# Kernel tuning notes

Hardware: AMD Instinct MI355X
Metric: run time of the kernel (lower is better)

## Reference

```python
import jax, jax.numpy as jnp
import numpy as np

B, S, E = 8, 2048, 2048   # batch, items, embedding_width
H, Dh = 16, 128           # head_width, head_embeddings (E = H*Dh)
M = 1024                  # memory_width


def setup_inputs() -> dict:
    key = jax.random.key(0)
    ks = jax.random.split(key, 9)
    scale_e = 1.0 / np.sqrt(E)
    scale_d = 1.0 / np.sqrt(Dh)
    return {
        "tensor": jax.random.normal(ks[0], (B, S, E), dtype=jnp.float32),
        # Query: Linear(E -> [H, Dh])
        "Wq": jax.random.normal(ks[1], (E, H, Dh), dtype=jnp.float32) * scale_e,
        "bq": jnp.zeros((H, Dh), dtype=jnp.float32),
        # trainable key/value banks + calibration (kaiming-uniform-like init)
        "key_params": (jax.random.uniform(ks[2], (H, M, Dh), dtype=jnp.float32) * 2 - 1) * np.sqrt(6.0 / Dh),
        "calibration": jnp.zeros((H, M, Dh), dtype=jnp.float32),
        "value": (jax.random.uniform(ks[3], (H, M, Dh), dtype=jnp.float32) * 2 - 1) * np.sqrt(6.0 / Dh),
        # Dehead: Linear([H, Dh] -> E)
        "Wd": jax.random.normal(ks[4], (H, Dh, E), dtype=jnp.float32) * scale_d,
        "bd": jnp.zeros((E,), dtype=jnp.float32),
    }


def reference(tensor, Wq, bq, key_params, calibration, value, Wd, bd):
    # query projection to heads: (B,S,E) -> (B,H,S,Dh) (fuses transpose(-2,-3))
    q = jnp.einsum("bse,ehd->bhsd", tensor, Wq) + bq[:, None, :]
    # eval-mode dropout is identity; key = KeyParameters + CalibrationBuffer
    k = key_params + calibration                      # (H,M,Dh)
    # scores scaled by sqrt(FULL embedding width), per the source
    score = jnp.einsum("bhsd,hmd->bhsm", q, k) / jnp.sqrt(jnp.float32(E))
    attn = jax.nn.softmax(score, axis=-1)             # (B,H,S,M)
    out = jnp.einsum("bhsm,hmd->bhsd", attn, value)   # (B,H,S,Dh)
    # dehead: (B,H,S,Dh) -> (B,S,E)
    return jnp.einsum("bhsd,hde->bse", out, Wd) + bd
```

## Files before the change

### kernel.cpp

```cpp
#include <hip/hip_runtime.h>
#include <stdint.h>

#define B_ 8
#define S_ 2048
#define E_ 2048
#define H_ 16
#define DH_ 128
#define M_ 1024
#define K_ 2048

typedef float f32x4 __attribute__((ext_vector_type(4)));
typedef float f32x16 __attribute__((ext_vector_type(16)));
typedef __bf16 bf16x8 __attribute__((ext_vector_type(8)));
typedef unsigned short ushort8 __attribute__((ext_vector_type(8)));
typedef unsigned short ushort4v __attribute__((ext_vector_type(4)));
typedef unsigned int uint4v __attribute__((ext_vector_type(4)));
typedef float float4v __attribute__((ext_vector_type(4)));

static __device__ __forceinline__ unsigned short f2bf(float f) {
  unsigned int u = __builtin_bit_cast(unsigned int, f);
  u += 0x7fffu + ((u >> 16) & 1u);
  return (unsigned short)(u >> 16);
}

static __device__ __forceinline__ float exp2f_fast(float x) {
#if __has_builtin(__builtin_amdgcn_exp2f)
  return __builtin_amdgcn_exp2f(x);
#else
  return __expf(x * 0.6931471805599453f);
#endif
}

static __device__ __forceinline__ f32x4 mfma16(ushort8 a, ushort8 b, f32x4 c) {
  return __builtin_amdgcn_mfma_f32_16x16x32_bf16(
      __builtin_bit_cast(bf16x8, a), __builtin_bit_cast(bf16x8, b), c, 0, 0, 0);
}

static __device__ __forceinline__ f32x16 mfma32(ushort8 a, ushort8 b, f32x16 c) {
  return __builtin_amdgcn_mfma_f32_32x32x16_bf16(
      __builtin_bit_cast(bf16x8, a), __builtin_bit_cast(bf16x8, b), c, 0, 0, 0);
}

static __device__ __forceinline__ void gload_lds16(const void* g, void* l) {
  __builtin_amdgcn_global_load_lds(
      (const __attribute__((address_space(1))) unsigned int*)g,
      (__attribute__((address_space(3))) unsigned int*)l, 16, 0, 0);
}


__global__ void cvt_bf16(const float* __restrict__ in, unsigned short* __restrict__ out, int n4) {
  int i = blockIdx.x * blockDim.x + threadIdx.x;
  int stride = gridDim.x * blockDim.x;
  for (; i < n4; i += stride) {
    float4v v = ((const float4v*)in)[i];
    ushort4v o;
    o[0] = f2bf(v[0]); o[1] = f2bf(v[1]); o[2] = f2bf(v[2]); o[3] = f2bf(v[3]);
    ((ushort4v*)out)[i] = o;
  }
}

__global__ void addcvt_bf16(const float* __restrict__ a, const float* __restrict__ b,
                            unsigned short* __restrict__ out, int n4) {
  int i = blockIdx.x * blockDim.x + threadIdx.x;
  int stride = gridDim.x * blockDim.x;
  for (; i < n4; i += stride) {
    float4v va = ((const float4v*)a)[i];
    float4v vb = ((const float4v*)b)[i];
    ushort4v o;
    o[0] = f2bf(va[0] + vb[0]); o[1] = f2bf(va[1] + vb[1]);
    o[2] = f2bf(va[2] + vb[2]); o[3] = f2bf(va[3] + vb[3]);
    ((ushort4v*)out)[i] = o;
  }
}

__global__ __launch_bounds__(256) void transpose_cvt(const float* __restrict__ in,
                                                     unsigned short* __restrict__ out,
                                                     int R, int C) {
  __shared__ float t[64][65];
  const int tx = threadIdx.x & 63, ty = threadIdx.x >> 6;
  const size_t base = (size_t)blockIdx.z * R * C;
  const int r0 = blockIdx.y * 64, c0 = blockIdx.x * 64;
#pragma unroll
  for (int i = 0; i < 64; i += 4)
    t[i + ty][tx] = in[base + (size_t)(r0 + i + ty) * C + (c0 + tx)];
  __syncthreads();
#pragma unroll
  for (int i = 0; i < 64; i += 4)
    out[base + (size_t)(c0 + i + ty) * R + (r0 + tx)] = f2bf(t[tx][i + ty]);
}

template <int EPI>
__global__ __launch_bounds__(512, 2) void gemm8p(const unsigned short* __restrict__ A,
                                                 const unsigned short* __restrict__ BT,
                                                 const float* __restrict__ bias,
                                                 void* __restrict__ Cout) {
  __shared__ __align__(16) unsigned short a_lds[2][2][8192];
  __shared__ __align__(16) unsigned short b_lds[2][2][8192];
  const int tid = threadIdx.x;
  const int w = tid >> 6, lane = tid & 63;
  const int l16 = lane & 15, l4 = lane >> 4;
  const int wr = w >> 2, wc = w & 3;
  const int bid = blockIdx.x;
  const int n0 = (bid & 7) << 8;
  const int m0 = (bid >> 3) << 8;

  const int rp0 = tid >> 3, gg0 = tid & 7, s0 = gg0 ^ (rp0 & 7);
  const int srow = rp0 * 2 + (s0 >> 2), sg = s0 & 3;
  const unsigned short* pA = A + (size_t)(m0 + srow) * K_ + sg * 8;
  const unsigned short* pB = BT + (size_t)(n0 + srow) * K_ + sg * 8;
  const int laneG = ((l16 >> 1) * 8 + (((l16 & 1) * 4 + l4) ^ ((l16 >> 1) & 7))) * 8;

  f32x4 acc[8][4];
#pragma unroll
  for (int i = 0; i < 8; ++i)
#pragma unroll
    for (int j = 0; j < 4; ++j) acc[i][j] = (f32x4)(0.f);

  ushort8 aF[4], bF[4];

#define STG(dst, srcp, T, kh)                                                \
  do {                                                                       \
    const unsigned short* s_ = (srcp) + (T) * 64 + (kh) * 32;                \
    gload_lds16(s_, &(dst)[tid * 8]);                                        \
    gload_lds16(s_ + (size_t)128 * K_, &(dst)[(512 + tid) * 8]);             \
  } while (0)

#define LDA(mg, buf, ks)                                                     \
  do {                                                                       \
    _Pragma("unroll") for (int mf = 0; mf < 4; ++mf)                         \
      aF[mf] = *(const ushort8*)&a_lds[buf][ks]                              \
          [(wr * 512 + ((mg) * 4 + mf) * 64) * 8 + laneG];                   \
  } while (0)

#define LDB(buf, ks)                                                         \
  do {                                                                       \
    _Pragma("unroll") for (int nf = 0; nf < 4; ++nf)                         \
      bF[nf] = *(const ushort8*)&b_lds[buf][ks]                              \
          [(wc * 256 + nf * 64) * 8 + laneG];                                \
  } while (0)

#define MM(mg)                                                               \
  do {                                                                       \
    __builtin_amdgcn_s_setprio(1);                                           \
    _Pragma("unroll") for (int mf = 0; mf < 4; ++mf)                         \
      _Pragma("unroll") for (int nf = 0; nf < 4; ++nf)                       \
        acc[(mg) * 4 + mf][nf] = mfma16(aF[mf], bF[nf], acc[(mg) * 4 + mf][nf]); \
    __builtin_amdgcn_s_setprio(0);                                           \
  } while (0)

#define NOVM ((void)0)
#define VMC6 asm volatile("s_waitcnt vmcnt(6)" ::: "memory")
#define VMC0 asm volatile("s_waitcnt vmcnt(0)" ::: "memory")

#define PHASE(mg, ks, buf, LOADB, STAGE, VM)                                 \
  do {                                                                       \
    if (LOADB) { LDB(buf, ks); }                                             \
    LDA(mg, buf, ks);                                                        \
    STAGE;                                                                   \
    __builtin_amdgcn_s_barrier();                                            \
    asm volatile("s_waitcnt lgkmcnt(0)" ::: "memory");                       \
    __builtin_amdgcn_sched_barrier(0);                                       \
    MM(mg);                                                                  \
    VM;                                                                      \
    __builtin_amdgcn_s_barrier();                                            \
  } while (0)

  STG(a_lds[0][0], pA, 0, 0);
  STG(b_lds[0][0], pB, 0, 0);
  STG(a_lds[0][1], pA, 0, 1);
  STG(b_lds[0][1], pB, 0, 1);
  STG(b_lds[1][0], pB, 1, 0);
  STG(a_lds[1][0], pA, 1, 0);
  STG(b_lds[1][1], pB, 1, 1);
  __builtin_amdgcn_sched_barrier(0);
  VMC6;
  __builtin_amdgcn_s_barrier();
  __builtin_amdgcn_sched_barrier(0);

#pragma unroll 1
  for (int i = 0; i < 15; ++i) {
    const int t1 = 2 * i + 1, t2 = 2 * i + 2, t3 = 2 * i + 3;
    PHASE(0, 0, 0, 1, STG(a_lds[1][1], pA, t1, 1), NOVM);
    PHASE(1, 0, 0, 0, STG(b_lds[0][0], pB, t2, 0), NOVM);
    PHASE(1, 1, 0, 1, STG(a_lds[0][0], pA, t2, 0), NOVM);
    PHASE(0, 1, 0, 0, STG(b_lds[0][1], pB, t2, 1), VMC6);
    PHASE(0, 0, 1, 1, STG(a_lds[0][1], pA, t2, 1), NOVM);
    PHASE(1, 0, 1, 0, STG(b_lds[1][0], pB, t3, 0), NOVM);
    PHASE(1, 1, 1, 1, STG(a_lds[1][0], pA, t3, 0), NOVM);
    PHASE(0, 1, 1, 0, STG(b_lds[1][1], pB, t3, 1), VMC6);
  }
  PHASE(0, 0, 0, 1, STG(a_lds[1][1], pA, 31, 1), NOVM);
  PHASE(1, 0, 0, 0, NOVM, NOVM);
  PHASE(1, 1, 0, 1, NOVM, NOVM);
  PHASE(0, 1, 0, 0, NOVM, VMC0);
  PHASE(0, 0, 1, 1, NOVM, NOVM);
  PHASE(1, 0, 1, 0, NOVM, NOVM);
  PHASE(1, 1, 1, 1, NOVM, NOVM);
  PHASE(0, 1, 1, 0, NOVM, NOVM);

#undef PHASE
#undef STG
#undef LDA
#undef LDB
#undef MM

#pragma unroll
  for (int mf = 0; mf < 8; ++mf) {
    const int mb = m0 + wr * 128 + mf * 16 + l4 * 4;
#pragma unroll
    for (int nf = 0; nf < 4; ++nf) {
      const int n = n0 + wc * 64 + nf * 16 + l16;
      const float bv = bias[n];
#pragma unroll
      for (int r = 0; r < 4; ++r) {
        const float v = acc[mf][nf][r] + bv;
        const int m = mb + r;
        if (EPI == 0) {
          const int b = m >> 11, s = m & 2047, h = n >> 7, d = n & 127;
          ((unsigned short*)Cout)[(((size_t)(b * 16 + h) << 11) + s) * 128 + d] =
              f2bf(v * 0.031879358f);
        } else {
          ((float*)Cout)[(size_t)m * E_ + n] = v;
        }
      }
    }
  }
}

__global__ __launch_bounds__(512, 2) void attnY(const unsigned short* __restrict__ Qb,
                                                const unsigned short* __restrict__ Kb,
                                                const unsigned short* __restrict__ VT,
                                                unsigned short* __restrict__ Ob) {
  const int bh = blockIdx.x, b = bh >> 4, h = bh & 15;
  const int tid = threadIdx.x, wv = tid >> 6, lane = tid & 63;
  const int l32 = lane & 31, hi = lane >> 5;
  const int rg = wv >> 1, dh = wv & 1;

  __shared__ __align__(16) unsigned short k_sm[2][16 * 512];
  __shared__ __align__(16) unsigned short v_sm[2][16 * 512];
  __shared__ float inv_lds[8][2][32];

  const unsigned short* Kh = Kb + (size_t)h * M_ * DH_;
  const unsigned short* Vh = VT + (size_t)h * DH_ * M_;

  ushort8 qf[2][8];
  const int srow0 = blockIdx.y * 256 + rg * 64;
#pragma unroll
  for (int sub = 0; sub < 2; ++sub) {
    const unsigned short* qrow =
        Qb + ((size_t)(b * 16 + h) * S_ + srow0 + sub * 32 + l32) * DH_ + hi * 8;
#pragma unroll
    for (int dc = 0; dc < 8; ++dc) qf[sub][dc] = *(const ushort8*)(qrow + dc * 16);
  }

  f32x16 oacc[2][2];
#pragma unroll
  for (int sub = 0; sub < 2; ++sub)
#pragma unroll
    for (int dt = 0; dt < 2; ++dt) oacc[sub][dt] = (f32x16)(0.f);
  float lsum[2] = {0.f, 0.f};

#define ASTAGE(buf, ch)                                                         \
  do {                                                                          \
    const int m0c = (ch) << 6;                                                  \
    _Pragma("unroll") for (int j_ = 0; j_ < 2; ++j_) {                          \
      const int L_ = j_ * 512 + tid;                                            \
      const int st_ = L_ >> 6, g_ = L_ & 63;                                    \
      const int mb_ = st_ >> 3, dc_ = st_ & 7;                                  \
      const int pt_ = g_ >> 5, rw_ = g_ & 31;                                   \
      gload_lds16(Kh + (size_t)(m0c + mb_ * 32 + rw_) * DH_ + dc_ * 16 + pt_ * 8, \
                  &k_sm[buf][L_ * 8]);                                          \
    }                                                                           \
    _Pragma("unroll") for (int j_ = 0; j_ < 2; ++j_) {                          \
      const int L_ = j_ * 512 + tid;                                            \
      const int st_ = L_ >> 6, g_ = L_ & 63;                                    \
      const int dt_ = st_ >> 2, mb_ = (st_ >> 1) & 1, mk_ = st_ & 1;            \
      const int pt_ = g_ >> 5, rw_ = g_ & 31;                                   \
      gload_lds16(Vh + (size_t)(dt_ * 32 + rw_) * M_ + m0c + mb_ * 32 + mk_ * 16 + pt_ * 8, \
                  &v_sm[buf][L_ * 8]);                                          \
    }                                                                           \
  } while (0)

  int cur = 0;
  ASTAGE(0, 0);
  __syncthreads();

  for (int c = 0; c < 16; ++c) {
    if (c < 15) ASTAGE(cur ^ 1, c + 1);

#pragma unroll
    for (int mb = 0; mb < 2; ++mb) {
      f32x16 sacc0 = (f32x16)(0.f), sacc1 = (f32x16)(0.f);
      __builtin_amdgcn_s_setprio(1);
#pragma unroll
      for (int dc = 0; dc < 8; ++dc) {
        ushort8 kf = *(const ushort8*)&k_sm[cur][((mb * 8 + dc) * 64 + lane) * 8];
        sacc0 = mfma32(kf, qf[0][dc], sacc0);
        sacc1 = mfma32(kf, qf[1][dc], sacc1);
      }
      __builtin_amdgcn_s_setprio(0);

      ushort8 pa[2][2];
#pragma unroll
      for (int sub = 0; sub < 2; ++sub) {
        float pe[16];
#pragma unroll
        for (int r = 0; r < 16; ++r) {
          pe[r] = exp2f_fast(sub == 0 ? sacc0[r] : sacc1[r]);
          lsum[sub] += pe[r];
        }
#pragma unroll
        for (int mk = 0; mk < 2; ++mk) {
          const int o = mk * 8;
          unsigned x0, x1, y0, y1;
          asm("v_cvt_pk_bf16_f32 %0, %1, %2" : "=v"(x0) : "v"(pe[o + 0]), "v"(pe[o + 1]));
          asm("v_cvt_pk_bf16_f32 %0, %1, %2" : "=v"(x1) : "v"(pe[o + 2]), "v"(pe[o + 3]));
          asm("v_cvt_pk_bf16_f32 %0, %1, %2" : "=v"(y0) : "v"(pe[o + 4]), "v"(pe[o + 5]));
          asm("v_cvt_pk_bf16_f32 %0, %1, %2" : "=v"(y1) : "v"(pe[o + 6]), "v"(pe[o + 7]));
          asm("v_permlane32_swap_b32 %0, %1" : "+v"(x0), "+v"(y0));
          asm("v_permlane32_swap_b32 %0, %1" : "+v"(x1), "+v"(y1));
          uint4v pw;
          pw[0] = x0; pw[1] = x1; pw[2] = y0; pw[3] = y1;
          pa[sub][mk] = __builtin_bit_cast(ushort8, pw);
        }
      }

      __builtin_amdgcn_s_setprio(1);
#pragma unroll
      for (int dt = 0; dt < 2; ++dt) {
#pragma unroll
        for (int mk = 0; mk < 2; ++mk) {
          const int vst = (dh * 2 + dt) * 4 + mb * 2 + mk;
          ushort8 vf = *(const ushort8*)&v_sm[cur][(vst * 64 + lane) * 8];
          oacc[0][dt] = mfma32(pa[0][mk], vf, oacc[0][dt]);
          oacc[1][dt] = mfma32(pa[1][mk], vf, oacc[1][dt]);
        }
      }
      __builtin_amdgcn_s_setprio(0);
    }
    __syncthreads();
    cur ^= 1;
  }
#undef ASTAGE

#pragma unroll
  for (int sub = 0; sub < 2; ++sub) {
    float tot = lsum[sub] + __shfl_xor(lsum[sub], 32, 64);
    if (hi == 0) inv_lds[wv][sub][l32] = 1.0f / tot;
  }
  __builtin_amdgcn_s_barrier();
#pragma unroll
  for (int sub = 0; sub < 2; ++sub)
#pragma unroll
    for (int r = 0; r < 16; ++r) {
      const int crow = (r & 3) + 8 * (r >> 2) + 4 * hi;
      const float iv = inv_lds[wv][sub][crow];
      unsigned short* orow =
          Ob + ((size_t)b * S_ + (size_t)(srow0 + sub * 32 + crow)) * (H_ * DH_) +
          h * DH_ + dh * 64 + l32;
#pragma unroll
      for (int dt = 0; dt < 2; ++dt) {
        const float val = oacc[sub][dt][r] * iv;
        unsigned u;
        asm("v_cvt_pk_bf16_f32 %0, %1, %2" : "=v"(u) : "v"(val), "v"(val));
        orow[dt * 32] = (unsigned short)u;
      }
    }
}


extern "C" void kernel_launch(void* const* d_in, const int* in_sizes, int n_in,
                              void* d_out, int out_size, void* d_ws, size_t ws_size,
                              hipStream_t stream) {
  const float* X   = (const float*)d_in[0];
  const float* Wq  = (const float*)d_in[1];
  const float* bq  = (const float*)d_in[2];
  const float* Kp  = (const float*)d_in[3];
  const float* Cal = (const float*)d_in[4];
  const float* V   = (const float*)d_in[5];
  const float* Wd  = (const float*)d_in[6];
  const float* bd  = (const float*)d_in[7];

  char* ws = (char*)d_ws;
  unsigned short* Xbf = (unsigned short*)(ws + 0);
  unsigned short* Ob  = Xbf;
  unsigned short* Qb  = (unsigned short*)(ws + 67108864);
  unsigned short* WqT = (unsigned short*)(ws + 134217728);
  unsigned short* WdT = (unsigned short*)(ws + 142606336);
  unsigned short* Kb  = (unsigned short*)(ws + 150994944);
  unsigned short* VT  = (unsigned short*)(ws + 155189248);

  cvt_bf16<<<2048, 256, 0, stream>>>(X, Xbf, (B_ * S_ * E_) / 4);
  addcvt_bf16<<<1024, 256, 0, stream>>>(Kp, Cal, Kb, (H_ * M_ * DH_) / 4);
  transpose_cvt<<<dim3(E_ / 64, E_ / 64, 1), 256, 0, stream>>>(Wq, WqT, E_, H_ * DH_);
  transpose_cvt<<<dim3(E_ / 64, E_ / 64, 1), 256, 0, stream>>>(Wd, WdT, H_ * DH_, E_);
  transpose_cvt<<<dim3(DH_ / 64, M_ / 64, H_), 256, 0, stream>>>(V, VT, M_, DH_);

  gemm8p<0><<<dim3(512), 512, 0, stream>>>(Xbf, WqT, bq, Qb);

  attnY<<<dim3(B_ * H_, S_ / 256), 512, 0, stream>>>(Qb, Kb, VT, Ob);

  gemm8p<1><<<dim3(512), 512, 0, stream>>>(Ob, WdT, bd, (float*)d_out);
}
```

Before: 574.6 us.

## Repartition attention waves to own full head dim, removing duplicated score computation

Each wave now owns 32 query rows across the full 128-wide head dimension, instead of 64 rows over half the head dimension. Previously two waves computed identical QK^T scores and exponentials for the same rows. The new split computes scores and softmax exponentials once per row. The trade is less register reuse of V fragments, since each V read now feeds one MFMA instead of two, so LDS traffic per output rises.

Result: faster. 509.3 us (-11.4%).

```diff
diff --git a/kernel.cpp b/kernel.cpp
--- a/kernel.cpp
+++ b/kernel.cpp
@@ -227,38 +227,33 @@
   }
 }
 
-__global__ __launch_bounds__(512, 2) void attnY(const unsigned short* __restrict__ Qb,
+__global__ __launch_bounds__(512, 2) void attnZ(const unsigned short* __restrict__ Qb,
                                                 const unsigned short* __restrict__ Kb,
                                                 const unsigned short* __restrict__ VT,
                                                 unsigned short* __restrict__ Ob) {
   const int bh = blockIdx.x, b = bh >> 4, h = bh & 15;
   const int tid = threadIdx.x, wv = tid >> 6, lane = tid & 63;
   const int l32 = lane & 31, hi = lane >> 5;
-  const int rg = wv >> 1, dh = wv & 1;
+  const int s_glob = blockIdx.y * 256 + wv * 32 + l32;
 
   __shared__ __align__(16) unsigned short k_sm[2][16 * 512];
   __shared__ __align__(16) unsigned short v_sm[2][16 * 512];
-  __shared__ float inv_lds[8][2][32];
+  __shared__ float inv_lds[8][32];
 
   const unsigned short* Kh = Kb + (size_t)h * M_ * DH_;
   const unsigned short* Vh = VT + (size_t)h * DH_ * M_;
 
-  ushort8 qf[2][8];
-  const int srow0 = blockIdx.y * 256 + rg * 64;
-#pragma unroll
-  for (int sub = 0; sub < 2; ++sub) {
-    const unsigned short* qrow =
-        Qb + ((size_t)(b * 16 + h) * S_ + srow0 + sub * 32 + l32) * DH_ + hi * 8;
-#pragma unroll
-    for (int dc = 0; dc < 8; ++dc) qf[sub][dc] = *(const ushort8*)(qrow + dc * 16);
-  }
-
-  f32x16 oacc[2][2];
-#pragma unroll
-  for (int sub = 0; sub < 2; ++sub)
-#pragma unroll
-    for (int dt = 0; dt < 2; ++dt) oacc[sub][dt] = (f32x16)(0.f);
-  float lsum[2] = {0.f, 0.f};
+  ushort8 qf[8];
+  {
+    const unsigned short* qrow = Qb + ((size_t)(b * 16 + h) * S_ + s_glob) * DH_ + hi * 8;
+#pragma unroll
+    for (int dc = 0; dc < 8; ++dc) qf[dc] = *(const ushort8*)(qrow + dc * 16);
+  }
+
+  f32x16 oacc[4];
+#pragma unroll
+  for (int dt = 0; dt < 4; ++dt) oacc[dt] = (f32x16)(0.f);
+  float lsum = 0.f;
 
 #define ASTAGE(buf, ch)                                                         \
   do {                                                                          \
@@ -290,50 +285,45 @@
 
 #pragma unroll
     for (int mb = 0; mb < 2; ++mb) {
-      f32x16 sacc0 = (f32x16)(0.f), sacc1 = (f32x16)(0.f);
+      f32x16 sacc = (f32x16)(0.f);
       __builtin_amdgcn_s_setprio(1);
 #pragma unroll
       for (int dc = 0; dc < 8; ++dc) {
         ushort8 kf = *(const ushort8*)&k_sm[cur][((mb * 8 + dc) * 64 + lane) * 8];
-        sacc0 = mfma32(kf, qf[0][dc], sacc0);
-        sacc1 = mfma32(kf, qf[1][dc], sacc1);
+        sacc = mfma32(kf, qf[dc], sacc);
       }
       __builtin_amdgcn_s_setprio(0);
 
-      ushort8 pa[2][2];
-#pragma unroll
-      for (int sub = 0; sub < 2; ++sub) {
-        float pe[16];
-#pragma unroll
-        for (int r = 0; r < 16; ++r) {
-          pe[r] = exp2f_fast(sub == 0 ? sacc0[r] : sacc1[r]);
-          lsum[sub] += pe[r];
-        }
+      float pe[16];
+#pragma unroll
+      for (int r = 0; r < 16; ++r) {
+        pe[r] = exp2f_fast(sacc[r]);
+        lsum += pe[r];
+      }
+      ushort8 pa[2];
+#pragma unroll
+      for (int mk = 0; mk < 2; ++mk) {
+        const int o = mk * 8;
+        unsigned x0, x1, y0, y1;
+        asm("v_cvt_pk_bf16_f32 %0, %1, %2" : "=v"(x0) : "v"(pe[o + 0]), "v"(pe[o + 1]));
+        asm("v_cvt_pk_bf16_f32 %0, %1, %2" : "=v"(x1) : "v"(pe[o + 2]), "v"(pe[o + 3]));
+        asm("v_cvt_pk_bf16_f32 %0, %1, %2" : "=v"(y0) : "v"(pe[o + 4]), "v"(pe[o + 5]));
+        asm("v_cvt_pk_bf16_f32 %0, %1, %2" : "=v"(y1) : "v"(pe[o + 6]), "v"(pe[o + 7]));
+        asm("v_permlane32_swap_b32 %0, %1" : "+v"(x0), "+v"(y0));
+        asm("v_permlane32_swap_b32 %0, %1" : "+v"(x1), "+v"(y1));
+        uint4v pw;
+        pw[0] = x0; pw[1] = x1; pw[2] = y0; pw[3] = y1;
+        pa[mk] = __builtin_bit_cast(ushort8, pw);
+      }
+
+      __builtin_amdgcn_s_setprio(1);
+#pragma unroll
+      for (int dt = 0; dt < 4; ++dt) {
 #pragma unroll
         for (int mk = 0; mk < 2; ++mk) {
-          const int o = mk * 8;
-          unsigned x0, x1, y0, y1;
-          asm("v_cvt_pk_bf16_f32 %0, %1, %2" : "=v"(x0) : "v"(pe[o + 0]), "v"(pe[o + 1]));
-          asm("v_cvt_pk_bf16_f32 %0, %1, %2" : "=v"(x1) : "v"(pe[o + 2]), "v"(pe[o + 3]));
-          asm("v_cvt_pk_bf16_f32 %0, %1, %2" : "=v"(y0) : "v"(pe[o + 4]), "v"(pe[o + 5]));
-          asm("v_cvt_pk_bf16_f32 %0, %1, %2" : "=v"(y1) : "v"(pe[o + 6]), "v"(pe[o + 7]));
-          asm("v_permlane32_swap_b32 %0, %1" : "+v"(x0), "+v"(y0));
-          asm("v_permlane32_swap_b32 %0, %1" : "+v"(x1), "+v"(y1));
-          uint4v pw;
-          pw[0] = x0; pw[1] = x1; pw[2] = y0; pw[3] = y1;
-          pa[sub][mk] = __builtin_bit_cast(ushort8, pw);
-        }
-      }
-
-      __builtin_amdgcn_s_setprio(1);
-#pragma unroll
-      for (int dt = 0; dt < 2; ++dt) {
-#pragma unroll
-        for (int mk = 0; mk < 2; ++mk) {
-          const int vst = (dh * 2 + dt) * 4 + mb * 2 + mk;
+          const int vst = dt * 4 + mb * 2 + mk;
           ushort8 vf = *(const ushort8*)&v_sm[cur][(vst * 64 + lane) * 8];
-          oacc[0][dt] = mfma32(pa[0][mk], vf, oacc[0][dt]);
-          oacc[1][dt] = mfma32(pa[1][mk], vf, oacc[1][dt]);
+          oacc[dt] = mfma32(pa[mk], vf, oacc[dt]);
         }
       }
       __builtin_amdgcn_s_setprio(0);
@@ -343,29 +333,24 @@
   }
 #undef ASTAGE
 
-#pragma unroll
-  for (int sub = 0; sub < 2; ++sub) {
-    float tot = lsum[sub] + __shfl_xor(lsum[sub], 32, 64);
-    if (hi == 0) inv_lds[wv][sub][l32] = 1.0f / tot;
-  }
+  float tot = lsum + __shfl_xor(lsum, 32, 64);
+  if (hi == 0) inv_lds[wv][l32] = 1.0f / tot;
   __builtin_amdgcn_s_barrier();
 #pragma unroll
-  for (int sub = 0; sub < 2; ++sub)
-#pragma unroll
-    for (int r = 0; r < 16; ++r) {
-      const int crow = (r & 3) + 8 * (r >> 2) + 4 * hi;
-      const float iv = inv_lds[wv][sub][crow];
-      unsigned short* orow =
-          Ob + ((size_t)b * S_ + (size_t)(srow0 + sub * 32 + crow)) * (H_ * DH_) +
-          h * DH_ + dh * 64 + l32;
-#pragma unroll
-      for (int dt = 0; dt < 2; ++dt) {
-        const float val = oacc[sub][dt][r] * iv;
-        unsigned u;
-        asm("v_cvt_pk_bf16_f32 %0, %1, %2" : "=v"(u) : "v"(val), "v"(val));
-        orow[dt * 32] = (unsigned short)u;
-      }
+  for (int r = 0; r < 16; ++r) {
+    const int crow = (r & 3) + 8 * (r >> 2) + 4 * hi;
+    const float iv = inv_lds[wv][crow];
+    unsigned short* orow =
+        Ob + ((size_t)b * S_ + (size_t)(blockIdx.y * 256 + wv * 32 + crow)) * (H_ * DH_) +
+        h * DH_ + l32;
+#pragma unroll
+    for (int dt = 0; dt < 4; ++dt) {
+      const float val = oacc[dt][r] * iv;
+      unsigned u;
+      asm("v_cvt_pk_bf16_f32 %0, %1, %2" : "=v"(u) : "v"(val), "v"(val));
+      orow[dt * 32] = (unsigned short)u;
     }
+  }
 }
 
 
@@ -398,7 +383,7 @@
 
   gemm8p<0><<<dim3(512), 512, 0, stream>>>(Xbf, WqT, bq, Qb);
 
-  attnY<<<dim3(B_ * H_, S_ / 256), 512, 0, stream>>>(Qb, Kb, VT, Ob);
+  attnZ<<<dim3(B_ * H_, S_ / 256), 512, 0, stream>>>(Qb, Kb, VT, Ob);
 
   gemm8p<1><<<dim3(512), 512, 0, stream>>>(Ob, WdT, bd, (float*)d_out);
 }
```
